# Optimization experiments

Measured on AMD Instinct MI355X. Metric: run time of the kernel, lower is better.

The kernel has to match this reference:

```python
import jax, jax.numpy as jnp
import numpy as np

BATCH, NUM_CENTERS, NUM_FEATURES = 8192, 2048, 512


def setup_inputs() -> dict:
    key = jax.random.key(0)
    k1, k2 = jax.random.split(key)
    inputs = jax.random.normal(k1, (BATCH, NUM_FEATURES), dtype=jnp.float32)
    centers = jax.random.normal(k2, (NUM_CENTERS, NUM_FEATURES), dtype=jnp.float32)
    sigmas = jnp.ones((NUM_CENTERS,), dtype=jnp.float32)
    return {"inputs": inputs, "centers": centers, "sigmas": sigmas}


def reference(inputs, centers, sigmas):
    # instead of materializing the [B, C, F] broadcast intermediate.
    x_sq = jnp.sum(inputs * inputs, axis=-1, keepdims=True)        # [B, 1]
    c_sq = jnp.sum(centers * centers, axis=-1)                     # [C]
    cross = jnp.einsum('bf,cf->bc', inputs, centers)               # [B, C]
    dists = x_sq + c_sq[None, :] - 2.0 * cross                     # [B, C]
    dists = jnp.maximum(dists, 0.0)  # guard tiny negatives from fp error
    return jnp.exp(-dists / (2.0 * sigmas * sigmas))               # [B, C]
```

## Files before the change

kernel.cpp:

```cpp
#include <hip/hip_runtime.h>
#include <hip/hip_bf16.h>
#include <stdint.h>


#define BATCH 8192
#define NCENT 2048
#define NFEAT 512

typedef float f32x4 __attribute__((ext_vector_type(4)));
typedef int   i32x8 __attribute__((ext_vector_type(8)));
typedef __bf16 bf16x8 __attribute__((ext_vector_type(8)));

union Frag8 {
    uint4 q[2];
    i32x8 v;
};
union FragAB {
    uint4 u;
    bf16x8 v;
};

static __device__ __forceinline__ unsigned int pack_bf16(float a, float b) {
    unsigned int ua = __builtin_bit_cast(unsigned int, a);
    unsigned int ub = __builtin_bit_cast(unsigned int, b);
    ua = (ua + 0x7fffu + ((ua >> 16) & 1u)) >> 16;
    ub = (ub + 0x7fffu + ((ub >> 16) & 1u)) >> 16;
    return ua | (ub << 16);
}

static __device__ __forceinline__ void llds16(const void* g, void* l) {
    __builtin_amdgcn_global_load_lds(
        (const __attribute__((address_space(1))) unsigned int*)g,
        (__attribute__((address_space(3))) unsigned int*)(uintptr_t)l,
        16, 0, 0);
}

__global__ __launch_bounds__(256) void convert_kernel(const float* __restrict__ X,
                                                      const float* __restrict__ Cn,
                                                      unsigned char* __restrict__ Xf8,
                                                      unsigned char* __restrict__ Cf8,
                                                      float* __restrict__ xsq,
                                                      float* __restrict__ csq) {
    const int bid  = blockIdx.x;
    const int lane = threadIdx.x & 63;
    const float* src;
    unsigned char* dst;
    float* nrm;
    int row;
    if (bid < BATCH / 4) {
        row = bid * 4 + (threadIdx.x >> 6);
        src = X; dst = Xf8; nrm = xsq;
    } else {
        row = (bid - BATCH / 4) * 4 + (threadIdx.x >> 6);
        src = Cn; dst = Cf8; nrm = csq;
    }
    const float4* p = (const float4*)(src + (size_t)row * NFEAT);
    float4 a = p[2 * lane];
    float4 b = p[2 * lane + 1];
    unsigned int lo = 0, hi = 0;
    lo = __builtin_amdgcn_cvt_pk_fp8_f32(a.x, a.y, lo, 0);
    lo = __builtin_amdgcn_cvt_pk_fp8_f32(a.z, a.w, lo, 1);
    hi = __builtin_amdgcn_cvt_pk_fp8_f32(b.x, b.y, hi, 0);
    hi = __builtin_amdgcn_cvt_pk_fp8_f32(b.z, b.w, hi, 1);
    ((uint2*)(dst + (size_t)row * NFEAT))[lane] = make_uint2(lo, hi);
    float s = a.x * a.x + a.y * a.y + a.z * a.z + a.w * a.w
            + b.x * b.x + b.y * b.y + b.z * b.z + b.w * b.w;
#pragma unroll
    for (int off = 32; off >= 1; off >>= 1) s += __shfl_down(s, off);
    if (lane == 0) nrm[row] = s;
}

__global__ __launch_bounds__(256) void rbf_gemm_fp8_kernel(
        const unsigned char* __restrict__ Xf8,
        const unsigned char* __restrict__ Cf8,
        const float* __restrict__ Sg,
        const float* __restrict__ xsq,
        const float* __restrict__ csq,
        float* __restrict__ out) {
    __shared__ unsigned char As[2][128 * 128];
    __shared__ unsigned char Bs[2][128 * 128];

    const int tid    = threadIdx.x;
    const int lane   = tid & 63;
    const int wave   = tid >> 6;
    const int wave_m = wave >> 1;
    const int wave_n = wave & 1;
    const int bm0 = blockIdx.y * 128;
    const int bn0 = blockIdx.x * 128;

    f32x4 acc[4][4];
#pragma unroll
    for (int i = 0; i < 4; ++i)
#pragma unroll
        for (int j = 0; j < 4; ++j) acc[i][j] = (f32x4){0.f, 0.f, 0.f, 0.f};

    const int fr   = lane & 15;
    const int quad = lane >> 4;

    auto stage = [&](int k0, int buf) {
#pragma unroll
        for (int i = 0; i < 4; ++i) {
            const int s   = (wave * 4 + i) * 64 + lane;
            const int row = s >> 3;
            const int c   = (s & 7) ^ (row & 7);
            llds16(Xf8 + (size_t)(bm0 + row) * NFEAT + k0 + c * 16,
                   As[buf] + (wave * 4 + i) * 1024);
            llds16(Cf8 + (size_t)(bn0 + row) * NFEAT + k0 + c * 16,
                   Bs[buf] + (wave * 4 + i) * 1024);
        }
    };

    stage(0, 0);
    __syncthreads();

#pragma unroll
    for (int kt = 0; kt < 4; ++kt) {
        const int p = kt & 1;
        if (kt < 3) stage((kt + 1) * 128, p ^ 1);

        Frag8 a[4], b[4];
#pragma unroll
        for (int mi = 0; mi < 4; ++mi) {
            const int row = wave_m * 64 + mi * 16 + fr;
            const unsigned char* base = As[p] + row * 128;
            a[mi].q[0] = *(const uint4*)(base + ((quad * 2 + 0) ^ (row & 7)) * 16);
            a[mi].q[1] = *(const uint4*)(base + ((quad * 2 + 1) ^ (row & 7)) * 16);
        }
#pragma unroll
        for (int nj = 0; nj < 4; ++nj) {
            const int row = wave_n * 64 + nj * 16 + fr;
            const unsigned char* base = Bs[p] + row * 128;
            b[nj].q[0] = *(const uint4*)(base + ((quad * 2 + 0) ^ (row & 7)) * 16);
            b[nj].q[1] = *(const uint4*)(base + ((quad * 2 + 1) ^ (row & 7)) * 16);
        }
#pragma unroll
        for (int mi = 0; mi < 4; ++mi)
#pragma unroll
            for (int nj = 0; nj < 4; ++nj)
                acc[mi][nj] = __builtin_amdgcn_mfma_scale_f32_16x16x128_f8f6f4(
                    a[mi].v, b[nj].v, acc[mi][nj],
                    0, 0,
                    0, 0x7F7F7F7F,
                    0, 0x7F7F7F7F);
        if (kt < 3) __syncthreads();
    }

    const int col = lane & 15;
    const int rq  = lane >> 4;
#pragma unroll
    for (int nj = 0; nj < 4; ++nj) {
        const int n      = bn0 + wave_n * 64 + nj * 16 + col;
        const float csqn = csq[n];
        const float sg   = Sg[n];
        const float inv  = 0.5f / (sg * sg);
#pragma unroll
        for (int mi = 0; mi < 4; ++mi) {
            const int mbase = bm0 + wave_m * 64 + mi * 16 + rq * 4;
#pragma unroll
            for (int r = 0; r < 4; ++r) {
                const int m = mbase + r;
                float d = xsq[m] + csqn - 2.0f * acc[mi][nj][r];
                d = fmaxf(d, 0.0f);
                __builtin_nontemporal_store(__expf(-d * inv),
                                            out + (size_t)m * NCENT + n);
            }
        }
    }
}

__global__ __launch_bounds__(256) void sumsq_kernel(const float* __restrict__ src,
                                                    float* __restrict__ dst) {
    const int row  = blockIdx.x * 4 + (threadIdx.x >> 6);
    const int lane = threadIdx.x & 63;
    const float4* p = (const float4*)(src + (size_t)row * NFEAT);
    float4 a = p[lane];
    float4 b = p[lane + 64];
    float s = a.x * a.x + a.y * a.y + a.z * a.z + a.w * a.w
            + b.x * b.x + b.y * b.y + b.z * b.z + b.w * b.w;
#pragma unroll
    for (int off = 32; off >= 1; off >>= 1) s += __shfl_down(s, off);
    if (lane == 0) dst[row] = s;
}

__global__ __launch_bounds__(256) void rbf_fallback_kernel(const float* __restrict__ X,
                                                           const float* __restrict__ Cn,
                                                           const float* __restrict__ Sg,
                                                           const float* __restrict__ xsq,
                                                           const float* __restrict__ csq,
                                                           float* __restrict__ out) {
    __shared__ unsigned int As[128 * 16];
    __shared__ unsigned int Bs[128 * 16];

    const int tid    = threadIdx.x;
    const int lane   = tid & 63;
    const int wave   = tid >> 6;
    const int wave_m = wave >> 1;
    const int wave_n = wave & 1;
    const int bm0 = blockIdx.y * 128;
    const int bn0 = blockIdx.x * 128;

    f32x4 acc[4][4];
#pragma unroll
    for (int i = 0; i < 4; ++i)
#pragma unroll
        for (int j = 0; j < 4; ++j) acc[i][j] = (f32x4){0.f, 0.f, 0.f, 0.f};

    for (int k0 = 0; k0 < NFEAT; k0 += 32) {
        __syncthreads();
#pragma unroll
        for (int j = 0; j < 4; ++j) {
            const int s    = j * 256 + tid;
            const int row  = s >> 3;
            const int col4 = s & 7;
            {
                const float4 f = *(const float4*)(X + (size_t)(bm0 + row) * NFEAT + k0 + col4 * 4);
                *(uint2*)&As[row * 16 + col4 * 2] =
                    make_uint2(pack_bf16(f.x, f.y), pack_bf16(f.z, f.w));
            }
            {
                const float4 f = *(const float4*)(Cn + (size_t)(bn0 + row) * NFEAT + k0 + col4 * 4);
                *(uint2*)&Bs[row * 16 + col4 * 2] =
                    make_uint2(pack_bf16(f.x, f.y), pack_bf16(f.z, f.w));
            }
        }
        __syncthreads();

        const int fr   = lane & 15;
        const int quad = lane >> 4;
        FragAB a[4], b[4];
#pragma unroll
        for (int mi = 0; mi < 4; ++mi)
            a[mi].u = *(const uint4*)&As[(wave_m * 64 + mi * 16 + fr) * 16 + quad * 4];
#pragma unroll
        for (int nj = 0; nj < 4; ++nj)
            b[nj].u = *(const uint4*)&Bs[(wave_n * 64 + nj * 16 + fr) * 16 + quad * 4];
#pragma unroll
        for (int mi = 0; mi < 4; ++mi)
#pragma unroll
            for (int nj = 0; nj < 4; ++nj)
                acc[mi][nj] = __builtin_amdgcn_mfma_f32_16x16x32_bf16(
                    a[mi].v, b[nj].v, acc[mi][nj], 0, 0, 0);
    }

    const int col = lane & 15;
    const int rq  = lane >> 4;
#pragma unroll
    for (int nj = 0; nj < 4; ++nj) {
        const int n      = bn0 + wave_n * 64 + nj * 16 + col;
        const float csqn = csq[n];
        const float sg   = Sg[n];
        const float inv  = 0.5f / (sg * sg);
#pragma unroll
        for (int mi = 0; mi < 4; ++mi) {
            const int mbase = bm0 + wave_m * 64 + mi * 16 + rq * 4;
#pragma unroll
            for (int r = 0; r < 4; ++r) {
                const int m = mbase + r;
                float d = xsq[m] + csqn - 2.0f * acc[mi][nj][r];
                d = fmaxf(d, 0.0f);
                out[(size_t)m * NCENT + n] = __expf(-d * inv);
            }
        }
    }
}

extern "C" void kernel_launch(void* const* d_in, const int* in_sizes, int n_in,
                              void* d_out, int out_size, void* d_ws, size_t ws_size,
                              hipStream_t stream) {
    const float* X  = (const float*)d_in[0];
    const float* Cn = (const float*)d_in[1];
    const float* Sg = (const float*)d_in[2];
    float* out = (float*)d_out;

    const size_t xb = (size_t)BATCH * NFEAT;
    const size_t cb = (size_t)NCENT * NFEAT;
    const size_t need = xb + cb + (size_t)(BATCH + NCENT) * 4;

    dim3 grid(NCENT / 128, BATCH / 128);

    if (ws_size >= need) {
        unsigned char* Xf8 = (unsigned char*)d_ws;
        unsigned char* Cf8 = Xf8 + xb;
        float* xsq = (float*)(Cf8 + cb);
        float* csq = xsq + BATCH;

        convert_kernel<<<(BATCH + NCENT) / 4, 256, 0, stream>>>(X, Cn, Xf8, Cf8, xsq, csq);
        rbf_gemm_fp8_kernel<<<grid, 256, 0, stream>>>(Xf8, Cf8, Sg, xsq, csq, out);
    } else {
        float* xsq = (float*)d_ws;
        float* csq = xsq + BATCH;
        sumsq_kernel<<<BATCH / 4, 256, 0, stream>>>(X, xsq);
        sumsq_kernel<<<NCENT / 4, 256, 0, stream>>>(Cn, csq);
        rbf_fallback_kernel<<<grid, 256, 0, stream>>>(X, Cn, Sg, xsq, csq, out);
    }
}
```

Before: 102.1 us.

## Pre-pack FP8 operands in MFMA fragment order and load directly from global

The convert kernel now writes X and centers in FP8 laid out in the exact per-lane MFMA fragment order, in 16-row blocks. The GEMM kernel then skips LDS staging, swizzling and barriers and reads each fragment straight from global memory with coalesced 16-byte loads. This removes shared-memory traffic and syncs. In exchange, data is no longer shared through LDS, so each wave pair re-reads the same operand fragments from L2/global, and there is no explicit prefetch or double buffering to hide latency.

```diff
diff --git a/kernel.cpp b/kernel.cpp
--- a/kernel.cpp
+++ b/kernel.cpp
@@ -28,58 +28,66 @@
     return ua | (ub << 16);
 }
 
-static __device__ __forceinline__ void llds16(const void* g, void* l) {
-    __builtin_amdgcn_global_load_lds(
-        (const __attribute__((address_space(1))) unsigned int*)g,
-        (__attribute__((address_space(3))) unsigned int*)(uintptr_t)l,
-        16, 0, 0);
-}
-
-__global__ __launch_bounds__(256) void convert_kernel(const float* __restrict__ X,
-                                                      const float* __restrict__ Cn,
-                                                      unsigned char* __restrict__ Xf8,
-                                                      unsigned char* __restrict__ Cf8,
-                                                      float* __restrict__ xsq,
-                                                      float* __restrict__ csq) {
-    const int bid  = blockIdx.x;
+__global__ __launch_bounds__(256) void convert_pack_kernel(
+        const float* __restrict__ X,
+        const float* __restrict__ Cn,
+        unsigned char* __restrict__ Apk,
+        unsigned char* __restrict__ Cpk,
+        float* __restrict__ xsq,
+        float* __restrict__ csq) {
+    const int wid  = blockIdx.x * 4 + (threadIdx.x >> 6);
     const int lane = threadIdx.x & 63;
+    const int q    = lane >> 4;
+    const int fr   = lane & 15;
+
     const float* src;
     unsigned char* dst;
     float* nrm;
-    int row;
-    if (bid < BATCH / 4) {
-        row = bid * 4 + (threadIdx.x >> 6);
-        src = X; dst = Xf8; nrm = xsq;
+    int rb;
+    if (wid < BATCH / 16) {
+        rb = wid;  src = X;  dst = Apk;  nrm = xsq;
     } else {
-        row = (bid - BATCH / 4) * 4 + (threadIdx.x >> 6);
-        src = Cn; dst = Cf8; nrm = csq;
-    }
+        rb = wid - BATCH / 16;  src = Cn;  dst = Cpk;  nrm = csq;
+    }
+    const int row = rb * 16 + fr;
     const float4* p = (const float4*)(src + (size_t)row * NFEAT);
-    float4 a = p[2 * lane];
-    float4 b = p[2 * lane + 1];
-    unsigned int lo = 0, hi = 0;
-    lo = __builtin_amdgcn_cvt_pk_fp8_f32(a.x, a.y, lo, 0);
-    lo = __builtin_amdgcn_cvt_pk_fp8_f32(a.z, a.w, lo, 1);
-    hi = __builtin_amdgcn_cvt_pk_fp8_f32(b.x, b.y, hi, 0);
-    hi = __builtin_amdgcn_cvt_pk_fp8_f32(b.z, b.w, hi, 1);
-    ((uint2*)(dst + (size_t)row * NFEAT))[lane] = make_uint2(lo, hi);
-    float s = a.x * a.x + a.y * a.y + a.z * a.z + a.w * a.w
-            + b.x * b.x + b.y * b.y + b.z * b.z + b.w * b.w;
-#pragma unroll
-    for (int off = 32; off >= 1; off >>= 1) s += __shfl_down(s, off);
-    if (lane == 0) nrm[row] = s;
+    unsigned char* ob = dst + (size_t)rb * 8192;
+
+    float s = 0.f;
+#pragma unroll
+    for (int kt = 0; kt < 4; ++kt) {
+        float4 f[8];
+#pragma unroll
+        for (int j = 0; j < 8; ++j) f[j] = p[(kt * 128 + q * 32) / 4 + j];
+        uint4 o0, o1;
+        unsigned int u;
+#pragma unroll
+        for (int h = 0; h < 2; ++h) {
+#pragma unroll
+            for (int w = 0; w < 4; ++w) {
+                const float4 g = f[h * 4 + w];
+                u = 0;
+                u = __builtin_amdgcn_cvt_pk_fp8_f32(g.x, g.y, u, 0);
+                u = __builtin_amdgcn_cvt_pk_fp8_f32(g.z, g.w, u, 1);
+                ((unsigned int*)(h ? &o1 : &o0))[w] = u;
+                s += g.x * g.x + g.y * g.y + g.z * g.z + g.w * g.w;
+            }
+        }
+        *(uint4*)(ob + (kt * 2 + 0) * 1024 + lane * 16) = o0;
+        *(uint4*)(ob + (kt * 2 + 1) * 1024 + lane * 16) = o1;
+    }
+    s += __shfl_xor(s, 16);
+    s += __shfl_xor(s, 32);
+    if (q == 0) nrm[row] = s;
 }
 
 __global__ __launch_bounds__(256) void rbf_gemm_fp8_kernel(
-        const unsigned char* __restrict__ Xf8,
-        const unsigned char* __restrict__ Cf8,
+        const unsigned char* __restrict__ Apk,
+        const unsigned char* __restrict__ Cpk,
         const float* __restrict__ Sg,
         const float* __restrict__ xsq,
         const float* __restrict__ csq,
         float* __restrict__ out) {
-    __shared__ unsigned char As[2][128 * 128];
-    __shared__ unsigned char Bs[2][128 * 128];
-
     const int tid    = threadIdx.x;
     const int lane   = tid & 63;
     const int wave   = tid >> 6;
@@ -88,50 +96,29 @@
     const int bm0 = blockIdx.y * 128;
     const int bn0 = blockIdx.x * 128;
 
+    const int m16b = blockIdx.y * 8 + wave_m * 4;
+    const int n16b = blockIdx.x * 8 + wave_n * 4;
+
     f32x4 acc[4][4];
 #pragma unroll
     for (int i = 0; i < 4; ++i)
 #pragma unroll
         for (int j = 0; j < 4; ++j) acc[i][j] = (f32x4){0.f, 0.f, 0.f, 0.f};
 
-    const int fr   = lane & 15;
-    const int quad = lane >> 4;
-
-    auto stage = [&](int k0, int buf) {
-#pragma unroll
-        for (int i = 0; i < 4; ++i) {
-            const int s   = (wave * 4 + i) * 64 + lane;
-            const int row = s >> 3;
-            const int c   = (s & 7) ^ (row & 7);
-            llds16(Xf8 + (size_t)(bm0 + row) * NFEAT + k0 + c * 16,
-                   As[buf] + (wave * 4 + i) * 1024);
-            llds16(Cf8 + (size_t)(bn0 + row) * NFEAT + k0 + c * 16,
-                   Bs[buf] + (wave * 4 + i) * 1024);
-        }
-    };
-
-    stage(0, 0);
-    __syncthreads();
-
-#pragma unroll
+    const unsigned char* abase = Apk + (size_t)m16b * 8192 + lane * 16;
+    const unsigned char* bbase = Cpk + (size_t)n16b * 8192 + lane * 16;
+
     for (int kt = 0; kt < 4; ++kt) {
-        const int p = kt & 1;
-        if (kt < 3) stage((kt + 1) * 128, p ^ 1);
-
         Frag8 a[4], b[4];
 #pragma unroll
         for (int mi = 0; mi < 4; ++mi) {
-            const int row = wave_m * 64 + mi * 16 + fr;
-            const unsigned char* base = As[p] + row * 128;
-            a[mi].q[0] = *(const uint4*)(base + ((quad * 2 + 0) ^ (row & 7)) * 16);
-            a[mi].q[1] = *(const uint4*)(base + ((quad * 2 + 1) ^ (row & 7)) * 16);
+            a[mi].q[0] = *(const uint4*)(abase + mi * 8192 + (kt * 2 + 0) * 1024);
+            a[mi].q[1] = *(const uint4*)(abase + mi * 8192 + (kt * 2 + 1) * 1024);
         }
 #pragma unroll
         for (int nj = 0; nj < 4; ++nj) {
-            const int row = wave_n * 64 + nj * 16 + fr;
-            const unsigned char* base = Bs[p] + row * 128;
-            b[nj].q[0] = *(const uint4*)(base + ((quad * 2 + 0) ^ (row & 7)) * 16);
-            b[nj].q[1] = *(const uint4*)(base + ((quad * 2 + 1) ^ (row & 7)) * 16);
+            b[nj].q[0] = *(const uint4*)(bbase + nj * 8192 + (kt * 2 + 0) * 1024);
+            b[nj].q[1] = *(const uint4*)(bbase + nj * 8192 + (kt * 2 + 1) * 1024);
         }
 #pragma unroll
         for (int mi = 0; mi < 4; ++mi)
@@ -142,7 +129,6 @@
                     0, 0,
                     0, 0x7F7F7F7F,
                     0, 0x7F7F7F7F);
-        if (kt < 3) __syncthreads();
     }
 
     const int col = lane & 15;
@@ -272,25 +258,26 @@
     const float* Sg = (const float*)d_in[2];
     float* out = (float*)d_out;
 
-    const size_t xb = (size_t)BATCH * NFEAT;
+    const size_t ab = (size_t)BATCH * NFEAT;
     const size_t cb = (size_t)NCENT * NFEAT;
-    const size_t need = xb + cb + (size_t)(BATCH + NCENT) * 4;
-
-    dim3 grid(NCENT / 128, BATCH / 128);
+    const size_t need = ab + cb + (size_t)(BATCH + NCENT) * 4;
 
     if (ws_size >= need) {
-        unsigned char* Xf8 = (unsigned char*)d_ws;
-        unsigned char* Cf8 = Xf8 + xb;
-        float* xsq = (float*)(Cf8 + cb);
+        unsigned char* Apk = (unsigned char*)d_ws;
+        unsigned char* Cpk = Apk + ab;
+        float* xsq = (float*)(Cpk + cb);
         float* csq = xsq + BATCH;
 
-        convert_kernel<<<(BATCH + NCENT) / 4, 256, 0, stream>>>(X, Cn, Xf8, Cf8, xsq, csq);
-        rbf_gemm_fp8_kernel<<<grid, 256, 0, stream>>>(Xf8, Cf8, Sg, xsq, csq, out);
+        convert_pack_kernel<<<(BATCH + NCENT) / 64, 256, 0, stream>>>(
+            X, Cn, Apk, Cpk, xsq, csq);
+        dim3 grid(NCENT / 128, BATCH / 128);
+        rbf_gemm_fp8_kernel<<<grid, 256, 0, stream>>>(Apk, Cpk, Sg, xsq, csq, out);
     } else {
         float* xsq = (float*)d_ws;
         float* csq = xsq + BATCH;
         sumsq_kernel<<<BATCH / 4, 256, 0, stream>>>(X, xsq);
         sumsq_kernel<<<NCENT / 4, 256, 0, stream>>>(Cn, csq);
+        dim3 grid(NCENT / 128, BATCH / 128);
         rbf_fallback_kernel<<<grid, 256, 0, stream>>>(X, Cn, Sg, xsq, csq, out);
     }
 }
```

New measurement: 109.6 us. 1.07x slower.
